# Kernel tuning notes

Hardware: AMD Instinct MI355X
Metric: run time of the kernel (lower is better)

The kernel has to match this reference:

```python
import jax, jax.numpy as jnp
import numpy as np

NUM_HEADS = 8
NUM_KEY_FEATURES = 128  # 32*1 + 32*3 (key fiber num_features)
N_NODES = 50000
N_EDGES = 500000
CH = 32  # value/key channels per degree


def setup_inputs() -> dict:
    key = jax.random.key(0)
    ks = jax.random.split(key, 7)
    return {
        "key0": jax.random.normal(ks[0], (N_EDGES, CH, 1), jnp.float32),
        "key1": jax.random.normal(ks[1], (N_EDGES, CH, 3), jnp.float32),
        "value0": jax.random.normal(ks[2], (N_EDGES, CH, 1), jnp.float32),
        "value1": jax.random.normal(ks[3], (N_EDGES, CH, 3), jnp.float32),
        "query0": jax.random.normal(ks[4], (N_NODES, CH, 1), jnp.float32),
        "query1": jax.random.normal(ks[5], (N_NODES, CH, 3), jnp.float32),
        "dst": jax.random.randint(ks[6], (N_EDGES,), 0, N_NODES, jnp.int64),
    }


def _to_heads(d0, d1):
    # Fiber.to_attention_heads: per-degree [*, C, 2d+1] -> [*, H, C//H*(2d+1)], concat over degrees
    a = d0.reshape(d0.shape[0], NUM_HEADS, -1)
    b = d1.reshape(d1.shape[0], NUM_HEADS, -1)
    return jnp.concatenate([a, b], axis=-1)  # [*, H, 16]


def reference(key0, key1, value0, value1, query0, query1, dst):
    n_nodes = query0.shape[0]
    k = _to_heads(key0, key1)      # [E, H, F]
    q = _to_heads(query0, query1)  # [N, H, F]
    # dgl.ops.e_dot_v: dot(key_e, query_{dst(e)}) per head
    logits = jnp.einsum('ehf,ehf->eh', k, q[dst]) / np.sqrt(NUM_KEY_FEATURES).astype(np.float32)
    # edge_softmax over incoming edges of each dst node
    m = jax.ops.segment_max(logits, dst, num_segments=n_nodes)       # [N, H]
    ex = jnp.exp(logits - m[dst])                                    # [E, H]
    s = jax.ops.segment_sum(ex, dst, num_segments=n_nodes)          # [N, H]
    w = ex / s[dst]                                                  # [E, H]

    def agg(v):
        e, c, dd = v.shape
        vh = v.reshape(e, NUM_HEADS, c // NUM_HEADS, dd)
        wv = w[:, :, None, None] * vh                                # [E, H, C/H, 2d+1]
        out = jax.ops.segment_sum(wv, dst, num_segments=n_nodes)
        return out.reshape(n_nodes, c, dd)                           # [N, C, 2d+1]

    return agg(value0), agg(value1)
```

## Files before the change

kernel.cpp:

```cpp
#include <hip/hip_runtime.h>
#include <hip/hip_bf16.h>
#include <math.h>

#define NHEADS 8
#define CHVAL 32
#define CAP 256
#define WPB 4

__global__ void scatter2_kernel(const int* __restrict__ dst,
                                int* __restrict__ cnt,
                                int* __restrict__ eid2,
                                int E) {
    int e = blockIdx.x * blockDim.x + threadIdx.x;
    if (e < E) {
        int n = dst[e];
        int c = atomicAdd(&cnt[n], 1);
        if (c < CAP) eid2[(size_t)n * CAP + c] = e;
    }
}

__global__ void logits2_kernel(const float4* __restrict__ key0,
                               const float4* __restrict__ key1,
                               const float4* __restrict__ q0,
                               const float4* __restrict__ q1,
                               const int* __restrict__ dst,
                               float* __restrict__ logits,
                               int EH2) {
    int tid = blockIdx.x * blockDim.x + threadIdx.x;
    if (tid >= EH2) return;
    const float SCALE = 0.08838834764831845f;

    int ta = tid, tb = tid + EH2;
    int ea = ta >> 3, ha = ta & 7;
    int eb = tb >> 3, hb = tb & 7;
    int qa_i = dst[ea] * 8 + ha;
    int qb_i = dst[eb] * 8 + hb;

    float4 ka0 = key0[ta];
    float4 kb0 = key0[tb];
    float4 qa0 = q0[qa_i];
    float4 qb0 = q0[qb_i];
    float4 ka1 = key1[ta * 3 + 0], ka2 = key1[ta * 3 + 1], ka3 = key1[ta * 3 + 2];
    float4 kb1 = key1[tb * 3 + 0], kb2 = key1[tb * 3 + 1], kb3 = key1[tb * 3 + 2];
    float4 qa1 = q1[qa_i * 3 + 0], qa2 = q1[qa_i * 3 + 1], qa3 = q1[qa_i * 3 + 2];
    float4 qb1 = q1[qb_i * 3 + 0], qb2 = q1[qb_i * 3 + 1], qb3 = q1[qb_i * 3 + 2];

    float da = ka0.x * qa0.x + ka0.y * qa0.y + ka0.z * qa0.z + ka0.w * qa0.w
             + ka1.x * qa1.x + ka1.y * qa1.y + ka1.z * qa1.z + ka1.w * qa1.w
             + ka2.x * qa2.x + ka2.y * qa2.y + ka2.z * qa2.z + ka2.w * qa2.w
             + ka3.x * qa3.x + ka3.y * qa3.y + ka3.z * qa3.z + ka3.w * qa3.w;
    float db = kb0.x * qb0.x + kb0.y * qb0.y + kb0.z * qb0.z + kb0.w * qb0.w
             + kb1.x * qb1.x + kb1.y * qb1.y + kb1.z * qb1.z + kb1.w * qb1.w
             + kb2.x * qb2.x + kb2.y * qb2.y + kb2.z * qb2.z + kb2.w * qb2.w
             + kb3.x * qb3.x + kb3.y * qb3.y + kb3.z * qb3.z + kb3.w * qb3.w;

    logits[ta] = da * SCALE;
    logits[tb] = db * SCALE;
}

__global__ void __launch_bounds__(64 * WPB)
node_kernel(const float* __restrict__ logits,
            const float4* __restrict__ value0,
            const float4* __restrict__ value1,
            const int* __restrict__ cnt,
            const int* __restrict__ eid2,
            float4* __restrict__ out0,
            float4* __restrict__ out1,
            int N) {
    __shared__ float w_sh[WPB][64][9];

    int wv = threadIdx.x >> 6;
    int t  = threadIdx.x & 63;
    int n  = blockIdx.x * WPB + wv;
    if (n >= N) return;

    const int* eidp = eid2 + (size_t)n * CAP;
    int deg = min(cnt[n], CAP);

    if (deg == 0) {
        float4 z = {0.f, 0.f, 0.f, 0.f};
        if (t < 8) out0[(size_t)n * 8 + t] = z;
        else if (t < 32) out1[(size_t)n * 24 + (t - 8)] = z;
        return;
    }

    int myeid = -1;
    float lg[8];
    if (t < deg) {
        myeid = eidp[t];
        const float4* lp = (const float4*)(logits + (size_t)myeid * 8);
        float4 a = lp[0], b = lp[1];
        lg[0] = a.x; lg[1] = a.y; lg[2] = a.z; lg[3] = a.w;
        lg[4] = b.x; lg[5] = b.y; lg[6] = b.z; lg[7] = b.w;
    } else {
#pragma unroll
        for (int k = 0; k < 8; ++k) lg[k] = -INFINITY;
    }

    float mx[8];
#pragma unroll
    for (int k = 0; k < 8; ++k) mx[k] = lg[k];
    for (int base = 64; base < deg; base += 64) {
        if (base + t < deg) {
            int e = eidp[base + t];
            const float4* lp = (const float4*)(logits + (size_t)e * 8);
            float4 a = lp[0], b = lp[1];
            float tt[8] = {a.x, a.y, a.z, a.w, b.x, b.y, b.z, b.w};
#pragma unroll
            for (int k = 0; k < 8; ++k) mx[k] = fmaxf(mx[k], tt[k]);
        }
    }
#pragma unroll
    for (int k = 0; k < 8; ++k)
        for (int off = 32; off; off >>= 1)
            mx[k] = fmaxf(mx[k], __shfl_xor(mx[k], off, 64));

    float ex0[8], sm[8];
#pragma unroll
    for (int k = 0; k < 8; ++k) { ex0[k] = __expf(lg[k] - mx[k]); sm[k] = ex0[k]; }
    for (int base = 64; base < deg; base += 64) {
        if (base + t < deg) {
            int e = eidp[base + t];
            const float4* lp = (const float4*)(logits + (size_t)e * 8);
            float4 a = lp[0], b = lp[1];
            float tt[8] = {a.x, a.y, a.z, a.w, b.x, b.y, b.z, b.w};
#pragma unroll
            for (int k = 0; k < 8; ++k) sm[k] += __expf(tt[k] - mx[k]);
        }
    }
#pragma unroll
    for (int k = 0; k < 8; ++k)
        for (int off = 32; off; off >>= 1)
            sm[k] += __shfl_xor(sm[k], off, 64);
    float inv[8];
#pragma unroll
    for (int k = 0; k < 8; ++k) inv[k] = 1.0f / sm[k];

    int half = t >> 5;
    int l = t & 31;
    int myh = (l < 8) ? l : ((l - 8) / 3);
    float4 acc = {0.f, 0.f, 0.f, 0.f};

    for (int base = 0; base < deg; base += 64) {
        int clen = min(64, deg - base);
        if (base == 0) {
            if (t < clen) {
#pragma unroll
                for (int k = 0; k < 8; ++k) w_sh[wv][t][k] = ex0[k] * inv[k];
            }
        } else {
            if (base + t < deg) {
                int e = eidp[base + t];
                const float4* lp = (const float4*)(logits + (size_t)e * 8);
                float4 a = lp[0], b = lp[1];
                float tt[8] = {a.x, a.y, a.z, a.w, b.x, b.y, b.z, b.w};
#pragma unroll
                for (int k = 0; k < 8; ++k)
                    w_sh[wv][t][k] = __expf(tt[k] - mx[k]) * inv[k];
            }
        }
        __builtin_amdgcn_wave_barrier();

        for (int ii = half; ii < clen; ii += 2) {
            int e = (base == 0) ? __shfl(myeid, ii, 64)
                                : eidp[base + ii];
            float w = w_sh[wv][ii][myh];
            float4 v = (l < 8) ? value0[(size_t)e * 8 + l]
                               : value1[(size_t)e * 24 + (l - 8)];
            acc.x += w * v.x;
            acc.y += w * v.y;
            acc.z += w * v.z;
            acc.w += w * v.w;
        }
        __builtin_amdgcn_wave_barrier();
    }

    acc.x += __shfl_xor(acc.x, 32, 64);
    acc.y += __shfl_xor(acc.y, 32, 64);
    acc.z += __shfl_xor(acc.z, 32, 64);
    acc.w += __shfl_xor(acc.w, 32, 64);
    if (t < 8)       out0[(size_t)n * 8 + l] = acc;
    else if (t < 32) out1[(size_t)n * 24 + (l - 8)] = acc;
}

extern "C" void kernel_launch(void* const* d_in, const int* in_sizes, int n_in,
                              void* d_out, int out_size, void* d_ws, size_t ws_size,
                              hipStream_t stream) {
    const float* key0   = (const float*)d_in[0];
    const float* key1   = (const float*)d_in[1];
    const float* value0 = (const float*)d_in[2];
    const float* value1 = (const float*)d_in[3];
    const float* query0 = (const float*)d_in[4];
    const float* query1 = (const float*)d_in[5];
    const int*   dst    = (const int*)d_in[6];

    int E = in_sizes[0] / CHVAL;
    int N = in_sizes[4] / CHVAL;
    int EH = E * NHEADS;
    int EH2 = EH / 2;

    float* logits = (float*)d_ws;
    int*   cnt    = (int*)(logits + EH);
    int*   eid2   = cnt + N;

    float* out0 = (float*)d_out;
    float* out1 = out0 + (size_t)N * 32;

    hipMemsetAsync(cnt, 0, (size_t)N * sizeof(int), stream);

    int blk = 256;
    scatter2_kernel<<<(E + blk - 1) / blk, blk, 0, stream>>>(dst, cnt, eid2, E);

    logits2_kernel<<<(EH2 + blk - 1) / blk, blk, 0, stream>>>(
        (const float4*)key0, (const float4*)key1,
        (const float4*)query0, (const float4*)query1,
        dst, logits, EH2);

    int nnb = (N + WPB - 1) / WPB;
    node_kernel<<<nnb, 64 * WPB, 0, stream>>>(logits,
                                              (const float4*)value0,
                                              (const float4*)value1,
                                              cnt, eid2,
                                              (float4*)out0, (float4*)out1, N);
}
```

Baseline: 186.0 us.

## Compute logits per destination node in CSR slot order

The logits kernel now runs per destination node instead of per edge. Each wave loads the query once and gathers its incoming edges' keys through the bucket list, writing logits into a per-node slot array. The node kernel then reads logits contiguously by slot rather than gathering them by edge id. The cost is random key gathers instead of streaming key reads, a much larger logits workspace (N*CAP*8 floats), and logits work that now waits on the scatter kernel.

```diff
diff --git a/kernel.cpp b/kernel.cpp
--- a/kernel.cpp
+++ b/kernel.cpp
@@ -19,43 +19,50 @@
     }
 }
 
-__global__ void logits2_kernel(const float4* __restrict__ key0,
-                               const float4* __restrict__ key1,
-                               const float4* __restrict__ q0,
-                               const float4* __restrict__ q1,
-                               const int* __restrict__ dst,
-                               float* __restrict__ logits,
-                               int EH2) {
-    int tid = blockIdx.x * blockDim.x + threadIdx.x;
-    if (tid >= EH2) return;
+__global__ void __launch_bounds__(64 * WPB)
+logits_csr2_kernel(const float4* __restrict__ key0,
+                   const float4* __restrict__ key1,
+                   const float4* __restrict__ q0,
+                   const float4* __restrict__ q1,
+                   const int* __restrict__ cnt,
+                   const int* __restrict__ eid2,
+                   float* __restrict__ logits,
+                   int N) {
+    int wv = threadIdx.x >> 6;
+    int t  = threadIdx.x & 63;
+    int n  = blockIdx.x * WPB + wv;
+    if (n >= N) return;
+
+    int deg = min(cnt[n], CAP);
+    if (deg == 0) return;
+
     const float SCALE = 0.08838834764831845f;
-
-    int ta = tid, tb = tid + EH2;
-    int ea = ta >> 3, ha = ta & 7;
-    int eb = tb >> 3, hb = tb & 7;
-    int qa_i = dst[ea] * 8 + ha;
-    int qb_i = dst[eb] * 8 + hb;
-
-    float4 ka0 = key0[ta];
-    float4 kb0 = key0[tb];
-    float4 qa0 = q0[qa_i];
-    float4 qb0 = q0[qb_i];
-    float4 ka1 = key1[ta * 3 + 0], ka2 = key1[ta * 3 + 1], ka3 = key1[ta * 3 + 2];
-    float4 kb1 = key1[tb * 3 + 0], kb2 = key1[tb * 3 + 1], kb3 = key1[tb * 3 + 2];
-    float4 qa1 = q1[qa_i * 3 + 0], qa2 = q1[qa_i * 3 + 1], qa3 = q1[qa_i * 3 + 2];
-    float4 qb1 = q1[qb_i * 3 + 0], qb2 = q1[qb_i * 3 + 1], qb3 = q1[qb_i * 3 + 2];
-
-    float da = ka0.x * qa0.x + ka0.y * qa0.y + ka0.z * qa0.z + ka0.w * qa0.w
-             + ka1.x * qa1.x + ka1.y * qa1.y + ka1.z * qa1.z + ka1.w * qa1.w
-             + ka2.x * qa2.x + ka2.y * qa2.y + ka2.z * qa2.z + ka2.w * qa2.w
-             + ka3.x * qa3.x + ka3.y * qa3.y + ka3.z * qa3.z + ka3.w * qa3.w;
-    float db = kb0.x * qb0.x + kb0.y * qb0.y + kb0.z * qb0.z + kb0.w * qb0.w
-             + kb1.x * qb1.x + kb1.y * qb1.y + kb1.z * qb1.z + kb1.w * qb1.w
-             + kb2.x * qb2.x + kb2.y * qb2.y + kb2.z * qb2.z + kb2.w * qb2.w
-             + kb3.x * qb3.x + kb3.y * qb3.y + kb3.z * qb3.z + kb3.w * qb3.w;
-
-    logits[ta] = da * SCALE;
-    logits[tb] = db * SCALE;
+    int s = t >> 3;
+    int h = t & 7;
+
+    const int* eidp = eid2 + (size_t)n * CAP;
+    float* lbase = logits + (size_t)n * CAP * 8;
+
+    float4 qa  = q0[(size_t)n * 8 + h];
+    float4 qb0 = q1[(size_t)n * 24 + 3 * h + 0];
+    float4 qb1 = q1[(size_t)n * 24 + 3 * h + 1];
+    float4 qb2 = q1[(size_t)n * 24 + 3 * h + 2];
+
+    for (int base = 0; base < deg; base += 8) {
+        int slot = base + s;
+        if (slot < deg) {
+            int e = eidp[slot];
+            float4 ka  = key0[(size_t)e * 8 + h];
+            float4 kb0 = key1[(size_t)e * 24 + 3 * h + 0];
+            float4 kb1 = key1[(size_t)e * 24 + 3 * h + 1];
+            float4 kb2 = key1[(size_t)e * 24 + 3 * h + 2];
+            float d = ka.x * qa.x + ka.y * qa.y + ka.z * qa.z + ka.w * qa.w
+                    + kb0.x * qb0.x + kb0.y * qb0.y + kb0.z * qb0.z + kb0.w * qb0.w
+                    + kb1.x * qb1.x + kb1.y * qb1.y + kb1.z * qb1.z + kb1.w * qb1.w
+                    + kb2.x * qb2.x + kb2.y * qb2.y + kb2.z * qb2.z + kb2.w * qb2.w;
+            lbase[(size_t)slot * 8 + h] = d * SCALE;
+        }
+    }
 }
 
 __global__ void __launch_bounds__(64 * WPB)
@@ -75,6 +82,7 @@
     if (n >= N) return;
 
     const int* eidp = eid2 + (size_t)n * CAP;
+    const float* lbase = logits + (size_t)n * CAP * 8;
     int deg = min(cnt[n], CAP);
 
     if (deg == 0) {
@@ -88,7 +96,7 @@
     float lg[8];
     if (t < deg) {
         myeid = eidp[t];
-        const float4* lp = (const float4*)(logits + (size_t)myeid * 8);
+        const float4* lp = (const float4*)(lbase + (size_t)t * 8);
         float4 a = lp[0], b = lp[1];
         lg[0] = a.x; lg[1] = a.y; lg[2] = a.z; lg[3] = a.w;
         lg[4] = b.x; lg[5] = b.y; lg[6] = b.z; lg[7] = b.w;
@@ -102,8 +110,7 @@
     for (int k = 0; k < 8; ++k) mx[k] = lg[k];
     for (int base = 64; base < deg; base += 64) {
         if (base + t < deg) {
-            int e = eidp[base + t];
-            const float4* lp = (const float4*)(logits + (size_t)e * 8);
+            const float4* lp = (const float4*)(lbase + (size_t)(base + t) * 8);
             float4 a = lp[0], b = lp[1];
             float tt[8] = {a.x, a.y, a.z, a.w, b.x, b.y, b.z, b.w};
 #pragma unroll
@@ -120,8 +127,7 @@
     for (int k = 0; k < 8; ++k) { ex0[k] = __expf(lg[k] - mx[k]); sm[k] = ex0[k]; }
     for (int base = 64; base < deg; base += 64) {
         if (base + t < deg) {
-            int e = eidp[base + t];
-            const float4* lp = (const float4*)(logits + (size_t)e * 8);
+            const float4* lp = (const float4*)(lbase + (size_t)(base + t) * 8);
             float4 a = lp[0], b = lp[1];
             float tt[8] = {a.x, a.y, a.z, a.w, b.x, b.y, b.z, b.w};
 #pragma unroll
@@ -150,8 +156,7 @@
             }
         } else {
             if (base + t < deg) {
-                int e = eidp[base + t];
-                const float4* lp = (const float4*)(logits + (size_t)e * 8);
+                const float4* lp = (const float4*)(lbase + (size_t)(base + t) * 8);
                 float4 a = lp[0], b = lp[1];
                 float tt[8] = {a.x, a.y, a.z, a.w, b.x, b.y, b.z, b.w};
 #pragma unroll
@@ -196,11 +201,9 @@
 
     int E = in_sizes[0] / CHVAL;
     int N = in_sizes[4] / CHVAL;
-    int EH = E * NHEADS;
-    int EH2 = EH / 2;
 
     float* logits = (float*)d_ws;
-    int*   cnt    = (int*)(logits + EH);
+    int*   cnt    = (int*)(logits + (size_t)N * CAP * 8);
     int*   eid2   = cnt + N;
 
     float* out0 = (float*)d_out;
@@ -211,12 +214,12 @@
     int blk = 256;
     scatter2_kernel<<<(E + blk - 1) / blk, blk, 0, stream>>>(dst, cnt, eid2, E);
 
-    logits2_kernel<<<(EH2 + blk - 1) / blk, blk, 0, stream>>>(
+    int nnb = (N + WPB - 1) / WPB;
+    logits_csr2_kernel<<<nnb, 64 * WPB, 0, stream>>>(
         (const float4*)key0, (const float4*)key1,
         (const float4*)query0, (const float4*)query1,
-        dst, logits, EH2);
-
-    int nnb = (N + WPB - 1) / WPB;
+        cnt, eid2, logits, N);
+
     node_kernel<<<nnb, 64 * WPB, 0, stream>>>(logits,
                                               (const float4*)value0,
                                               (const float4*)value1,
```

Result: faster. 178.8 us (-3.9%).
